# Kernel optimization log

Hardware: AMD Instinct MI355X
Metric: run time of the kernel (lower is better)

The kernel has to match this reference:

```python
import jax, jax.numpy as jnp
import numpy as np

B, S, D = 4, 2048, 1024
N_HEAD = 16
HEAD_DIM = D // N_HEAD


def setup_inputs() -> dict:
    key = jax.random.key(0)
    k1, k2, k3 = jax.random.split(key, 3)
    std = 0.02
    return {
        "x": jax.random.normal(k1, (B, S, D), dtype=jnp.float32),
        "c_attn_w": jax.random.normal(k2, (D, 3 * D), dtype=jnp.float32) * std,
        "c_attn_b": jnp.zeros((3 * D,), dtype=jnp.float32),
        "c_proj_w": jax.random.normal(k3, (D, D), dtype=jnp.float32) * std,
        "c_proj_b": jnp.zeros((D,), dtype=jnp.float32),
    }


def _split_heads(t):
    # [B, S, D] -> [B, H, S, hd]
    b, s, d = t.shape
    return t.reshape(b, s, N_HEAD, d // N_HEAD).transpose(0, 2, 1, 3)


def reference(x, c_attn_w, c_attn_b, c_proj_w, c_proj_b):
    # fused QKV projection (TFConv1D = x @ w + b)
    qkv = x @ c_attn_w + c_attn_b                      # [B, S, 3D]
    q, k, v = jnp.split(qkv, 3, axis=2)
    q, k, v = _split_heads(q), _split_heads(k), _split_heads(v)  # [B, H, S, hd]

    # scaled scores
    w = jnp.einsum('bhqd,bhkd->bhqk', q, k)
    w = w / jnp.sqrt(jnp.asarray(HEAD_DIM, w.dtype))

    # causal mask via multiplicative trick: i >= j - ns + nd (nd == ns == S)
    nd = ns = S
    i = jnp.arange(nd)[:, None]
    j = jnp.arange(ns)[None, :]
    b = (i >= j - ns + nd).astype(w.dtype)[None, None]  # [1,1,nd,ns]
    w = w * b - 10000.0 * (1.0 - b)

    w = jax.nn.softmax(w, axis=-1)
    a = jnp.einsum('bhqk,bhkd->bhqd', w, v)            # [B, H, S, hd]

    # merge heads: [B, H, S, hd] -> [B, S, D]
    a = a.transpose(0, 2, 1, 3).reshape(x.shape[0], x.shape[1], -1)
    a = a @ c_proj_w + c_proj_b
    return a
```

## Files before the change

### kernel.cpp

```cpp
#include <hip/hip_runtime.h>
#include <hip/hip_bf16.h>

typedef unsigned short ushort_t;
typedef __attribute__((ext_vector_type(8))) short short8;
typedef __attribute__((ext_vector_type(4))) float floatx4;

#define LOG2E 1.4426950408889634f

__device__ __forceinline__ unsigned short f2bf(float f) {
    unsigned u = __float_as_uint(f);
    u += 0x7FFF + ((u >> 16) & 1);
    return (unsigned short)(u >> 16);
}

__device__ __forceinline__ void async_ld16(const void* gptr, void* lptr) {
    typedef const __attribute__((address_space(1))) unsigned int TG;
    typedef __attribute__((address_space(3))) unsigned int TL;
    __builtin_amdgcn_global_load_lds((TG*)(unsigned long long)gptr,
                                     (TL*)(unsigned)(unsigned long long)lptr,
                                     16, 0, 0);
}

__global__ __launch_bounds__(256) void prep_kernel(const float* __restrict__ x,
                                                   const float* __restrict__ wqkv,
                                                   const float* __restrict__ wproj,
                                                   ushort_t* __restrict__ xb,
                                                   ushort_t* __restrict__ wqkvT,
                                                   ushort_t* __restrict__ wprojT) {
    __shared__ float t[32][33];
    int bx = blockIdx.x;
    if (bx < 8192) {
        int i = bx * 256 + threadIdx.x;
        float4 v = ((const float4*)x)[i];
        unsigned long long r = (unsigned long long)f2bf(v.x)
                             | ((unsigned long long)f2bf(v.y) << 16)
                             | ((unsigned long long)f2bf(v.z) << 32)
                             | ((unsigned long long)f2bf(v.w) << 48);
        ((unsigned long long*)xb)[i] = r;
        return;
    }
    const float* in; ushort_t* out; int R, C, bidx;
    if (bx < 8192 + 3072) { in = wqkv; out = wqkvT; R = 1024; C = 3072; bidx = bx - 8192; }
    else                  { in = wproj; out = wprojT; R = 1024; C = 1024; bidx = bx - 11264; }
    int nbc = C >> 5;
    int bc = bidx % nbc, br = bidx / nbc;
    int tx = threadIdx.x & 31, ty = threadIdx.x >> 5;
    int r0 = br << 5, c0 = bc << 5;
#pragma unroll
    for (int j = 0; j < 4; ++j)
        t[ty + j * 8][tx] = in[(size_t)(r0 + ty + j * 8) * C + c0 + tx];
    __syncthreads();
#pragma unroll
    for (int j = 0; j < 4; ++j)
        out[(size_t)(c0 + ty + j * 8) * R + r0 + tx] = f2bf(t[tx][ty + j * 8]);
}

__global__ __launch_bounds__(512) void gemm_qkv_kernel(const ushort_t* __restrict__ A,
                                                       const ushort_t* __restrict__ Bt,
                                                       const float* __restrict__ bias,
                                                       ushort_t* __restrict__ qbuf,
                                                       ushort_t* __restrict__ kbuf,
                                                       ushort_t* __restrict__ vtbuf) {
    extern __shared__ __align__(16) ushort_t lds[];

    int bid = blockIdx.x;
    int wg = (bid & 7) * 48 + (bid >> 3);
    int bm = wg & 31, bn = wg >> 5;
    int m0 = bm << 8, n0 = bn << 8;

    int tid = threadIdx.x;
    int wave = tid >> 6, lane = tid & 63;
    int c = lane & 15, g = lane >> 4;
    int wm = wave >> 2, wn = wave & 3;

    int row0 = tid >> 3;
    int sch  = (tid & 7) ^ (row0 & 7);
    size_t aoff = (size_t)(m0 + row0) * 1024 + sch * 8;
    size_t boff = (size_t)(n0 + row0) * 1024 + sch * 8;

    int co0 = (g * 8) ^ ((c & 7) << 3);
    int co1 = co0 ^ 32;
    int Ab0 = wm * 8192,                 Ab1 = Ab0 + 16384;
    int Bb0 = 32768 + (wn >> 1) * 8192,  Bb1 = Bb0 + 16384;
    int bcol = (wn & 1) * 64;

    floatx4 acc[8][4];
    short8 a[4][2], b0f[2][2], b1f[2][2];
#pragma unroll
    for (int i2 = 0; i2 < 8; ++i2)
#pragma unroll
        for (int j2 = 0; j2 < 4; ++j2) { floatx4 z = {0.f,0.f,0.f,0.f}; acc[i2][j2] = z; }

    auto stA = [&](int t, int h, int buf) {
        const ushort_t* s = A + aoff + (size_t)h * 131072 + (size_t)t * 64;
        ushort_t* d = lds + buf * 16384 + h * 8192 + tid * 8;
        async_ld16(s, d);
        async_ld16(s + 65536, d + 4096);
    };
    auto stB = [&](int t, int h, int buf) {
        const ushort_t* s = Bt + boff + (size_t)h * 131072 + (size_t)t * 64;
        ushort_t* d = lds + 32768 + buf * 16384 + h * 8192 + tid * 8;
        async_ld16(s, d);
        async_ld16(s + 65536, d + 4096);
    };
    auto ld_a = [&](int abase, int qm) {
#pragma unroll
        for (int mi = 0; mi < 4; ++mi) {
            int ro = abase + (qm * 64 + mi * 16 + c) * 64;
            a[mi][0] = *(const short8*)&lds[ro + co0];
            a[mi][1] = *(const short8*)&lds[ro + co1];
        }
    };
    auto ld_b = [&](int bbase, int qn, short8 (&bf)[2][2]) {
#pragma unroll
        for (int nii = 0; nii < 2; ++nii) {
            int ro = bbase + (bcol + (qn * 2 + nii) * 16 + c) * 64;
            bf[nii][0] = *(const short8*)&lds[ro + co0];
            bf[nii][1] = *(const short8*)&lds[ro + co1];
        }
    };
    auto phase_mm = [&](int qm, int qn, short8 (&bf)[2][2]) {
        asm volatile("s_barrier" ::: "memory");
        asm volatile("s_waitcnt lgkmcnt(0)" ::: "memory");
        __builtin_amdgcn_s_setprio(1);
#pragma unroll
        for (int mi = 0; mi < 4; ++mi)
#pragma unroll
            for (int nii = 0; nii < 2; ++nii)
#pragma unroll
                for (int ks = 0; ks < 2; ++ks)
                    acc[qm * 4 + mi][qn * 2 + nii] =
                        __builtin_amdgcn_mfma_f32_16x16x32_bf16(
                            a[mi][ks], bf[nii][ks], acc[qm * 4 + mi][qn * 2 + nii], 0, 0, 0);
        __builtin_amdgcn_s_setprio(0);
        asm volatile("s_barrier" ::: "memory");
    };

    stA(0, 0, 0); stA(0, 1, 0); stB(0, 0, 0); stB(0, 1, 0);
    stA(1, 0, 1); stB(1, 0, 1); stB(1, 1, 1);
    asm volatile("s_waitcnt vmcnt(6)" ::: "memory");
    asm volatile("s_barrier" ::: "memory");

#pragma unroll 1
    for (int i = 0; i < 7; ++i) {
        int t0 = 2 * i;
        ld_a(Ab0, 0); ld_b(Bb0, 0, b0f);
        stA(t0 + 1, 1, 1);
        phase_mm(0, 0, b0f);
        ld_b(Bb0, 1, b1f);
        stB(t0 + 2, 0, 0);
        phase_mm(0, 1, b1f);
        ld_a(Ab0, 1);
        stB(t0 + 2, 1, 0);
        phase_mm(1, 1, b1f);
        stA(t0 + 2, 0, 0);
        asm volatile("s_waitcnt vmcnt(6)" ::: "memory");
        phase_mm(1, 0, b0f);
        ld_a(Ab1, 0); ld_b(Bb1, 0, b0f);
        stA(t0 + 2, 1, 0);
        phase_mm(0, 0, b0f);
        ld_b(Bb1, 1, b1f);
        stB(t0 + 3, 0, 1);
        phase_mm(0, 1, b1f);
        ld_a(Ab1, 1);
        stB(t0 + 3, 1, 1);
        phase_mm(1, 1, b1f);
        stA(t0 + 3, 0, 1);
        asm volatile("s_waitcnt vmcnt(6)" ::: "memory");
        phase_mm(1, 0, b0f);
    }
    ld_a(Ab0, 0); ld_b(Bb0, 0, b0f);
    stA(15, 1, 1);
    phase_mm(0, 0, b0f);
    ld_b(Bb0, 1, b1f);
    phase_mm(0, 1, b1f);
    ld_a(Ab0, 1);
    phase_mm(1, 1, b1f);
    asm volatile("s_waitcnt vmcnt(0)" ::: "memory");
    phase_mm(1, 0, b0f);
    ld_a(Ab1, 0); ld_b(Bb1, 0, b0f);
    phase_mm(0, 0, b0f);
    ld_b(Bb1, 1, b1f);
    phase_mm(0, 1, b1f);
    ld_a(Ab1, 1);
    phase_mm(1, 1, b1f);
    phase_mm(1, 0, b0f);

    int sec = n0 >> 10;
    int h0 = (n0 & 1023) >> 6;
    int b  = m0 >> 11, sbase = m0 & 2047;
    int bh0 = b * 16 + h0;
    float bv[4];
#pragma unroll
    for (int ni = 0; ni < 4; ++ni) bv[ni] = bias[n0 + wn * 64 + ni * 16 + c];

    __syncthreads();

    if (sec < 2) {
        float scl = (sec == 0) ? (0.125f * LOG2E) : 1.0f;
#pragma unroll
        for (int mi8 = 0; mi8 < 8; ++mi8) {
            int sr0 = wm * 128 + (mi8 >> 2) * 64 + (mi8 & 3) * 16 + g * 4;
#pragma unroll
            for (int ni = 0; ni < 4; ++ni)
#pragma unroll
                for (int r = 0; r < 4; ++r)
                    lds[wn * 18432 + (sr0 + r) * 72 + ni * 16 + c] =
                        f2bf((acc[mi8][ni][r] + bv[ni]) * scl);
        }
        __syncthreads();
        ushort_t* dst = (sec == 0 ? qbuf : kbuf)
                      + (size_t)(bh0 + (wave & 3)) * 131072
                      + (size_t)(sbase + (wave >> 2) * 128) * 64;
        const ushort_t* srcb = lds + (wave & 3) * 18432 + (wave >> 2) * 128 * 72;
#pragma unroll
        for (int j = 0; j < 16; ++j) {
            int e = j * 512 + lane * 8;
            *(short8*)(dst + e) =
                *(const short8*)(srcb + (e >> 6) * 72 + (lane & 7) * 8);
        }
    } else {
#pragma unroll
        for (int mi8 = 0; mi8 < 8; ++mi8) {
            int s0 = wm * 128 + (mi8 >> 2) * 64 + (mi8 & 3) * 16 + g * 4;
#pragma unroll
            for (int ni = 0; ni < 4; ++ni) {
                int d = ni * 16 + c;
                unsigned long long pk =
                      (unsigned long long)f2bf(acc[mi8][ni][0] + bv[ni])
                    | ((unsigned long long)f2bf(acc[mi8][ni][1] + bv[ni]) << 16)
                    | ((unsigned long long)f2bf(acc[mi8][ni][2] + bv[ni]) << 32)
                    | ((unsigned long long)f2bf(acc[mi8][ni][3] + bv[ni]) << 48);
                *(unsigned long long*)&lds[wn * 16896 + d * 264 + s0] = pk;
            }
        }
        __syncthreads();
        const ushort_t* srcb = lds + (wave & 3) * 16896 + (wave >> 2) * 32 * 264;
        ushort_t* dstb = vtbuf + (size_t)(bh0 + (wave & 3)) * 131072
                       + (size_t)((wave >> 2) * 32) * 2048 + sbase;
#pragma unroll
        for (int j = 0; j < 16; ++j) {
            int e = j * 512 + lane * 8;
            int d = e >> 8, sc = e & 255;
            *(short8*)(dstb + (size_t)d * 2048 + sc) =
                *(const short8*)(srcb + d * 264 + sc);
        }
    }
}

__global__ __launch_bounds__(256, 5) void attn_kernel(const ushort_t* __restrict__ qb_,
                                                      const ushort_t* __restrict__ kb_,
                                                      const ushort_t* __restrict__ vtb_,
                                                      ushort_t* __restrict__ aout) {
    __shared__ __align__(16) ushort_t Ks[64 * 68];
    __shared__ __align__(16) ushort_t Vs[64 * 68];
    __shared__ __align__(16) ushort_t Ps[4][16 * 68];
    int bx = blockIdx.x;
    int qb = 31 - (bx >> 6);
    int bhix = bx & 63;
    int b = bhix >> 4, h = bhix & 15;
    int q0 = qb << 6;
    int tid = threadIdx.x, wave = tid >> 6, lane = tid & 63;
    int c = lane & 15, g = lane >> 4;
    size_t bh = (size_t)(b * 16 + h);

    const ushort_t* Qp = qb_ + (bh * 2048 + q0) * 64;
    const ushort_t* Kp = kb_ + bh * 131072;
    const ushort_t* Vp = vtb_ + bh * 131072;

    int qr = wave * 16 + c;
    short8 qf0 = *(const short8*)(Qp + qr * 64 + g * 8);
    short8 qf1 = *(const short8*)(Qp + qr * 64 + 32 + g * 8);

    float l_part = 0.f;
    floatx4 o_acc[4];
#pragma unroll
    for (int nt = 0; nt < 4; ++nt) { floatx4 z = {0.f,0.f,0.f,0.f}; o_acc[nt] = z; }

    short8 kreg[2], vreg[2];
#pragma unroll
    for (int it = 0; it < 2; ++it) {
        int idx = it * 256 + tid;
        kreg[it] = *(const short8*)(Kp + idx * 8);
        vreg[it] = *(const short8*)(Vp + (idx >> 3) * 2048 + (idx & 7) * 8);
    }

    int qg = q0 + wave * 16 + c;
    for (int kt = 0; kt <= qb; ++kt) {
        int kt0 = kt << 6;
        __syncthreads();
#pragma unroll
        for (int it = 0; it < 2; ++it) {
            int idx = it * 256 + tid;
            *(short8*)&Ks[(idx >> 3) * 68 + (idx & 7) * 8] = kreg[it];
            *(short8*)&Vs[(idx >> 3) * 68 + (idx & 7) * 8] = vreg[it];
        }
        __syncthreads();
        if (kt < qb) {
            int s0 = (kt + 1) << 6;
#pragma unroll
            for (int it = 0; it < 2; ++it) {
                int idx = it * 256 + tid;
                kreg[it] = *(const short8*)(Kp + s0 * 64 + idx * 8);
                vreg[it] = *(const short8*)(Vp + (idx >> 3) * 2048 + s0 + (idx & 7) * 8);
            }
        }
        bool diag = (kt == qb);

        float lp = 0.f;
#pragma unroll
        for (int nt = 0; nt < 4; ++nt) {
            short8 kf0 = *(const short8*)&Ks[(nt * 16 + c) * 68 + g * 8];
            short8 kf1 = *(const short8*)&Ks[(nt * 16 + c) * 68 + 32 + g * 8];
            floatx4 z = {0.f, 0.f, 0.f, 0.f};
            z = __builtin_amdgcn_mfma_f32_16x16x32_bf16(kf0, qf0, z, 0, 0, 0);
            z = __builtin_amdgcn_mfma_f32_16x16x32_bf16(kf1, qf1, z, 0, 0, 0);

            int kpb = kt0 + nt * 16 + g * 4;
            float p[4];
#pragma unroll
            for (int r = 0; r < 4; ++r) {
                float s = z[r];
                if (diag) s = (kpb + r > qg) ? -1e30f : s;
                p[r] = exp2f(s);
                lp += p[r];
            }
            union { unsigned long long u; __hip_bfloat162 h2[2]; } pk;
            pk.h2[0] = __float22bfloat162_rn(make_float2(p[0], p[1]));
            pk.h2[1] = __float22bfloat162_rn(make_float2(p[2], p[3]));
            *(unsigned long long*)&Ps[wave][c * 68 + nt * 16 + g * 4] = pk.u;
        }
        l_part += lp;

#pragma unroll
        for (int ks = 0; ks < 2; ++ks) {
            short8 pf = *(const short8*)&Ps[wave][c * 68 + ks * 32 + g * 8];
#pragma unroll
            for (int nt = 0; nt < 4; ++nt) {
                short8 vf = *(const short8*)&Vs[(nt * 16 + c) * 68 + ks * 32 + g * 8];
                o_acc[nt] = __builtin_amdgcn_mfma_f32_16x16x32_bf16(pf, vf, o_acc[nt], 0, 0, 0);
            }
        }
    }

    float l = l_part;
    l += __shfl_xor(l, 16);
    l += __shfl_xor(l, 32);
    float linv = 1.0f / l;
    float inv[4];
#pragma unroll
    for (int r = 0; r < 4; ++r)
        inv[r] = __shfl(linv, g * 4 + r);
#pragma unroll
    for (int nt = 0; nt < 4; ++nt)
#pragma unroll
        for (int r = 0; r < 4; ++r) {
            int q = q0 + wave * 16 + g * 4 + r;
            aout[(size_t)(b * 2048 + q) * 1024 + h * 64 + nt * 16 + c] =
                f2bf(o_acc[nt][r] * inv[r]);
        }
}

__global__ __launch_bounds__(256) void gemm_proj_kernel(const ushort_t* __restrict__ A,
                                                        const ushort_t* __restrict__ Bt,
                                                        const float* __restrict__ bias,
                                                        float* __restrict__ Cout) {
    const int K = 1024, N = 1024, nbn = 8;
    __shared__ __align__(16) ushort_t As[128 * 32];
    __shared__ __align__(16) ushort_t Bs[128 * 32];
    int bm = blockIdx.x / nbn, bn = blockIdx.x % nbn;
    int m0 = bm << 7, n0 = bn << 7;
    int tid = threadIdx.x;
    int wave = tid >> 6, lane = tid & 63;
    int c = lane & 15, g = lane >> 4;
    int m_off = (wave & 1) << 6, n_off = (wave >> 1) << 6;
    int ldrow = lane >> 2;
    int ldk   = (lane & 3) << 3;

    floatx4 acc[4][4];
#pragma unroll
    for (int mi = 0; mi < 4; ++mi)
#pragma unroll
        for (int ni = 0; ni < 4; ++ni) {
            floatx4 z = {0.f, 0.f, 0.f, 0.f};
            acc[mi][ni] = z;
        }

    for (int kk = 0; kk < K; kk += 32) {
        __syncthreads();
#pragma unroll
        for (int j = 0; j < 2; ++j) {
            int chunk = wave * 2 + j;
            async_ld16(A  + (size_t)(m0 + chunk * 16 + ldrow) * K + kk + ldk, &As[chunk * 512]);
            async_ld16(Bt + (size_t)(n0 + chunk * 16 + ldrow) * K + kk + ldk, &Bs[chunk * 512]);
        }
        __syncthreads();
        short8 bf[4];
#pragma unroll
        for (int ni = 0; ni < 4; ++ni)
            bf[ni] = *(const short8*)&Bs[(n_off + ni * 16 + c) * 32 + g * 8];
#pragma unroll
        for (int mi = 0; mi < 4; ++mi) {
            short8 af = *(const short8*)&As[(m_off + mi * 16 + c) * 32 + g * 8];
#pragma unroll
            for (int ni = 0; ni < 4; ++ni)
                acc[mi][ni] = __builtin_amdgcn_mfma_f32_16x16x32_bf16(af, bf[ni], acc[mi][ni], 0, 0, 0);
        }
    }

    float bv[4];
#pragma unroll
    for (int ni = 0; ni < 4; ++ni) bv[ni] = bias[n0 + n_off + ni * 16 + c];
#pragma unroll
    for (int mi = 0; mi < 4; ++mi)
#pragma unroll
        for (int ni = 0; ni < 4; ++ni)
#pragma unroll
            for (int r = 0; r < 4; ++r) {
                int row = m0 + m_off + mi * 16 + g * 4 + r;
                int col = n0 + n_off + ni * 16 + c;
                Cout[(size_t)row * N + col] = acc[mi][ni][r] + bv[ni];
            }
}

extern "C" void kernel_launch(void* const* d_in, const int* in_sizes, int n_in,
                              void* d_out, int out_size, void* d_ws, size_t ws_size,
                              hipStream_t stream) {
    const float* x        = (const float*)d_in[0];
    const float* c_attn_w = (const float*)d_in[1];
    const float* c_attn_b = (const float*)d_in[2];
    const float* c_proj_w = (const float*)d_in[3];
    const float* c_proj_b = (const float*)d_in[4];
    float* out = (float*)d_out;

    char* ws = (char*)d_ws;
    ushort_t* xb     = (ushort_t*)(ws);
    ushort_t* wqkvT  = (ushort_t*)(ws + 16777216);
    ushort_t* wprojT = (ushort_t*)(ws + 23068672);
    ushort_t* qbuf   = (ushort_t*)(ws + 25165824);
    ushort_t* kbuf   = (ushort_t*)(ws + 41943040);
    ushort_t* vtbuf  = (ushort_t*)(ws + 58720256);

    static bool s_attr_set = false;
    if (!s_attr_set) {
        (void)hipFuncSetAttribute(reinterpret_cast<const void*>(gemm_qkv_kernel),
                                  hipFuncAttributeMaxDynamicSharedMemorySize, 147456);
        s_attr_set = true;
    }

    prep_kernel<<<12288, 256, 0, stream>>>(x, c_attn_w, c_proj_w, xb, wqkvT, wprojT);
    gemm_qkv_kernel<<<384, 512, 147456, stream>>>(xb, wqkvT, c_attn_b, qbuf, kbuf, vtbuf);
    attn_kernel<<<2048, 256, 0, stream>>>(qbuf, kbuf, vtbuf, xb);
    gemm_proj_kernel<<<64 * 8, 256, 0, stream>>>(xb, wprojT, c_proj_b, out);
}
```

Before: 256.2 us.

## Process two 64-row query tiles per attention block to reuse K/V tiles

Each attention block now handles 128 query rows as two 64-row sub-tiles sharing every K/V tile loaded into LDS, halving the grid to 1024 blocks. This is meant to cut global K/V loads and LDS staging per query row. Block order changes from heaviest-first to interleaved query blocks within each head, and register pressure grows, so the occupancy hint drops from 5 to 4 blocks per CU. The extra accumulators and the per-tile branch for the first sub-tile may reduce latency hiding and worsen load balance.

```diff
diff --git a/kernel.cpp b/kernel.cpp
--- a/kernel.cpp
+++ b/kernel.cpp
@@ -248,18 +248,18 @@
     }
 }
 
-__global__ __launch_bounds__(256, 5) void attn_kernel(const ushort_t* __restrict__ qb_,
+__global__ __launch_bounds__(256, 4) void attn_kernel(const ushort_t* __restrict__ qb_,
                                                       const ushort_t* __restrict__ kb_,
                                                       const ushort_t* __restrict__ vtb_,
                                                       ushort_t* __restrict__ aout) {
     __shared__ __align__(16) ushort_t Ks[64 * 68];
     __shared__ __align__(16) ushort_t Vs[64 * 68];
-    __shared__ __align__(16) ushort_t Ps[4][16 * 68];
+    __shared__ __align__(16) ushort_t Ps[4][2][16 * 68];
     int bx = blockIdx.x;
-    int qb = 31 - (bx >> 6);
-    int bhix = bx & 63;
+    int qb2 = bx & 15;
+    int bhix = bx >> 4;
     int b = bhix >> 4, h = bhix & 15;
-    int q0 = qb << 6;
+    int q0 = qb2 << 7;
     int tid = threadIdx.x, wave = tid >> 6, lane = tid & 63;
     int c = lane & 15, g = lane >> 4;
     size_t bh = (size_t)(b * 16 + h);
@@ -269,13 +269,18 @@
     const ushort_t* Vp = vtb_ + bh * 131072;
 
     int qr = wave * 16 + c;
-    short8 qf0 = *(const short8*)(Qp + qr * 64 + g * 8);
-    short8 qf1 = *(const short8*)(Qp + qr * 64 + 32 + g * 8);
-
-    float l_part = 0.f;
-    floatx4 o_acc[4];
-#pragma unroll
-    for (int nt = 0; nt < 4; ++nt) { floatx4 z = {0.f,0.f,0.f,0.f}; o_acc[nt] = z; }
+    short8 qf0a = *(const short8*)(Qp + qr * 64 + g * 8);
+    short8 qf1a = *(const short8*)(Qp + qr * 64 + 32 + g * 8);
+    short8 qf0b = *(const short8*)(Qp + (64 + qr) * 64 + g * 8);
+    short8 qf1b = *(const short8*)(Qp + (64 + qr) * 64 + 32 + g * 8);
+
+    float l0 = 0.f, l1 = 0.f;
+    floatx4 oa[4], ob[4];
+#pragma unroll
+    for (int nt = 0; nt < 4; ++nt) {
+        floatx4 z = {0.f,0.f,0.f,0.f};
+        oa[nt] = z; ob[nt] = z;
+    }
 
     short8 kreg[2], vreg[2];
 #pragma unroll
@@ -285,8 +290,11 @@
         vreg[it] = *(const short8*)(Vp + (idx >> 3) * 2048 + (idx & 7) * 8);
     }
 
-    int qg = q0 + wave * 16 + c;
-    for (int kt = 0; kt <= qb; ++kt) {
+    int qg0 = q0 + qr;
+    int qg1 = qg0 + 64;
+    int nkt = 2 * qb2 + 2;
+
+    for (int kt = 0; kt < nkt; ++kt) {
         int kt0 = kt << 6;
         __syncthreads();
 #pragma unroll
@@ -296,7 +304,7 @@
             *(short8*)&Vs[(idx >> 3) * 68 + (idx & 7) * 8] = vreg[it];
         }
         __syncthreads();
-        if (kt < qb) {
+        if (kt + 1 < nkt) {
             int s0 = (kt + 1) << 6;
 #pragma unroll
             for (int it = 0; it < 2; ++it) {
@@ -305,60 +313,91 @@
                 vreg[it] = *(const short8*)(Vp + (idx >> 3) * 2048 + s0 + (idx & 7) * 8);
             }
         }
-        bool diag = (kt == qb);
-
-        float lp = 0.f;
+        bool act0  = (kt < nkt - 1);
+        bool diag0 = (kt == nkt - 2);
+        bool diag1 = (kt == nkt - 1);
+
+        float lp0 = 0.f, lp1 = 0.f;
 #pragma unroll
         for (int nt = 0; nt < 4; ++nt) {
             short8 kf0 = *(const short8*)&Ks[(nt * 16 + c) * 68 + g * 8];
             short8 kf1 = *(const short8*)&Ks[(nt * 16 + c) * 68 + 32 + g * 8];
-            floatx4 z = {0.f, 0.f, 0.f, 0.f};
-            z = __builtin_amdgcn_mfma_f32_16x16x32_bf16(kf0, qf0, z, 0, 0, 0);
-            z = __builtin_amdgcn_mfma_f32_16x16x32_bf16(kf1, qf1, z, 0, 0, 0);
-
             int kpb = kt0 + nt * 16 + g * 4;
-            float p[4];
-#pragma unroll
-            for (int r = 0; r < 4; ++r) {
-                float s = z[r];
-                if (diag) s = (kpb + r > qg) ? -1e30f : s;
-                p[r] = exp2f(s);
-                lp += p[r];
-            }
-            union { unsigned long long u; __hip_bfloat162 h2[2]; } pk;
-            pk.h2[0] = __float22bfloat162_rn(make_float2(p[0], p[1]));
-            pk.h2[1] = __float22bfloat162_rn(make_float2(p[2], p[3]));
-            *(unsigned long long*)&Ps[wave][c * 68 + nt * 16 + g * 4] = pk.u;
-        }
-        l_part += lp;
+
+            floatx4 zb = {0.f, 0.f, 0.f, 0.f};
+            zb = __builtin_amdgcn_mfma_f32_16x16x32_bf16(kf0, qf0b, zb, 0, 0, 0);
+            zb = __builtin_amdgcn_mfma_f32_16x16x32_bf16(kf1, qf1b, zb, 0, 0, 0);
+
+            if (act0) {
+                floatx4 za = {0.f, 0.f, 0.f, 0.f};
+                za = __builtin_amdgcn_mfma_f32_16x16x32_bf16(kf0, qf0a, za, 0, 0, 0);
+                za = __builtin_amdgcn_mfma_f32_16x16x32_bf16(kf1, qf1a, za, 0, 0, 0);
+                float p[4];
+#pragma unroll
+                for (int r = 0; r < 4; ++r) {
+                    float s = za[r];
+                    if (diag0) s = (kpb + r > qg0) ? -1e30f : s;
+                    p[r] = exp2f(s);
+                    lp0 += p[r];
+                }
+                union { unsigned long long u; __hip_bfloat162 h2[2]; } pk;
+                pk.h2[0] = __float22bfloat162_rn(make_float2(p[0], p[1]));
+                pk.h2[1] = __float22bfloat162_rn(make_float2(p[2], p[3]));
+                *(unsigned long long*)&Ps[wave][0][c * 68 + nt * 16 + g * 4] = pk.u;
+            }
+            {
+                float p[4];
+#pragma unroll
+                for (int r = 0; r < 4; ++r) {
+                    float s = zb[r];
+                    if (diag1) s = (kpb + r > qg1) ? -1e30f : s;
+                    p[r] = exp2f(s);
+                    lp1 += p[r];
+                }
+                union { unsigned long long u; __hip_bfloat162 h2[2]; } pk;
+                pk.h2[0] = __float22bfloat162_rn(make_float2(p[0], p[1]));
+                pk.h2[1] = __float22bfloat162_rn(make_float2(p[2], p[3]));
+                *(unsigned long long*)&Ps[wave][1][c * 68 + nt * 16 + g * 4] = pk.u;
+            }
+        }
+        l0 += lp0;
+        l1 += lp1;
 
 #pragma unroll
         for (int ks = 0; ks < 2; ++ks) {
-            short8 pf = *(const short8*)&Ps[wave][c * 68 + ks * 32 + g * 8];
+            short8 pfa, pfb;
+            if (act0) pfa = *(const short8*)&Ps[wave][0][c * 68 + ks * 32 + g * 8];
+            pfb = *(const short8*)&Ps[wave][1][c * 68 + ks * 32 + g * 8];
 #pragma unroll
             for (int nt = 0; nt < 4; ++nt) {
                 short8 vf = *(const short8*)&Vs[(nt * 16 + c) * 68 + ks * 32 + g * 8];
-                o_acc[nt] = __builtin_amdgcn_mfma_f32_16x16x32_bf16(pf, vf, o_acc[nt], 0, 0, 0);
-            }
-        }
-    }
-
-    float l = l_part;
-    l += __shfl_xor(l, 16);
-    l += __shfl_xor(l, 32);
-    float linv = 1.0f / l;
-    float inv[4];
-#pragma unroll
-    for (int r = 0; r < 4; ++r)
-        inv[r] = __shfl(linv, g * 4 + r);
-#pragma unroll
-    for (int nt = 0; nt < 4; ++nt)
-#pragma unroll
-        for (int r = 0; r < 4; ++r) {
-            int q = q0 + wave * 16 + g * 4 + r;
-            aout[(size_t)(b * 2048 + q) * 1024 + h * 64 + nt * 16 + c] =
-                f2bf(o_acc[nt][r] * inv[r]);
-        }
+                if (act0) oa[nt] = __builtin_amdgcn_mfma_f32_16x16x32_bf16(pfa, vf, oa[nt], 0, 0, 0);
+                ob[nt] = __builtin_amdgcn_mfma_f32_16x16x32_bf16(pfb, vf, ob[nt], 0, 0, 0);
+            }
+        }
+    }
+
+#pragma unroll
+    for (int st = 0; st < 2; ++st) {
+        float l = st ? l1 : l0;
+        l += __shfl_xor(l, 16);
+        l += __shfl_xor(l, 32);
+        float linv = 1.0f / l;
+        float inv[4];
+#pragma unroll
+        for (int r = 0; r < 4; ++r)
+            inv[r] = __shfl(linv, g * 4 + r);
+        floatx4* oacc = st ? ob : oa;
+        int qsb = q0 + st * 64 + wave * 16 + g * 4;
+#pragma unroll
+        for (int nt = 0; nt < 4; ++nt)
+#pragma unroll
+            for (int r = 0; r < 4; ++r) {
+                int q = qsb + r;
+                aout[(size_t)(b * 2048 + q) * 1024 + h * 64 + nt * 16 + c] =
+                    f2bf(oacc[nt][r] * inv[r]);
+            }
+    }
 }
 
 __global__ __launch_bounds__(256) void gemm_proj_kernel(const ushort_t* __restrict__ A,
@@ -450,6 +489,6 @@
 
     prep_kernel<<<12288, 256, 0, stream>>>(x, c_attn_w, c_proj_w, xb, wqkvT, wprojT);
     gemm_qkv_kernel<<<384, 512, 147456, stream>>>(xb, wqkvT, c_attn_b, qbuf, kbuf, vtbuf);
-    attn_kernel<<<2048, 256, 0, stream>>>(qbuf, kbuf, vtbuf, xb);
+    attn_kernel<<<1024, 256, 0, stream>>>(qbuf, kbuf, vtbuf, xb);
     gemm_proj_kernel<<<64 * 8, 256, 0, stream>>>(xb, wprojT, c_proj_b, out);
 }
```

Result: slower. 304.9 us (+19.0%).
